# Performance work log

Hardware: AMD Instinct MI355X
Metric: run time of the kernel (lower is better)

The kernel has to match this reference:

```python
import jax, jax.numpy as jnp
import numpy as np

N = 50000
D = 256
E = 800000


def setup_inputs() -> dict:
    key = jax.random.key(0)
    ks = jax.random.split(key, 9)
    X = jax.random.normal(ks[0], (N, D), dtype=jnp.float32)
    edge_index = jax.random.randint(ks[1], (2, E), 0, N, dtype=jnp.int32)
    edge_weight = jax.random.uniform(ks[2], (E,), dtype=jnp.float32)
    p = jax.random.normal(ks[3], (D,), dtype=jnp.float32)
    s = 1.0 / np.sqrt(D)
    W_ih = jax.random.normal(ks[4], (3 * D, D), dtype=jnp.float32) * s
    W_hh = jax.random.normal(ks[5], (3 * D, D), dtype=jnp.float32) * s
    b_ih = jax.random.normal(ks[6], (3 * D,), dtype=jnp.float32) * s
    b_hh = jax.random.normal(ks[7], (3 * D,), dtype=jnp.float32) * s
    W0 = jax.random.normal(ks[8], (D, D), dtype=jnp.float32) * s
    return {"X": X, "edge_index": edge_index, "edge_weight": edge_weight,
            "p": p, "W_ih": W_ih, "W_hh": W_hh, "b_ih": b_ih, "b_hh": b_hh, "W0": W0}


def reference(X, edge_index, edge_weight, p, W_ih, W_hh, b_ih, b_hh, W0):
    n, d = X.shape  # n=N, d=D; ratio = d/n -> TopK keeps k=d nodes
    k = d

    # ---- TopKPooling: score = X.p/||p||, keep top-k, gate by tanh(score) ----
    score = X @ p / jnp.linalg.norm(p)          # [n]
    top_score, idx = jax.lax.top_k(score, k)    # [k]
    x_tilde = X[idx] * jnp.tanh(top_score)[:, None]  # [k, d]

    # ---- Single-step GRU: input x_tilde (batch=k=d), hidden = conv weight W0 [d,d] ----
    h = W0
    gi = x_tilde @ W_ih.T + b_ih                # [d, 3d]
    gh = h @ W_hh.T + b_hh                      # [d, 3d]
    i_r, i_z, i_n = jnp.split(gi, 3, axis=1)
    h_r, h_z, h_n = jnp.split(gh, 3, axis=1)
    r = jax.nn.sigmoid(i_r + h_r)
    z = jax.nn.sigmoid(i_z + h_z)
    nn_ = jnp.tanh(i_n + r * h_n)
    W_new = (1.0 - z) * nn_ + z * h             # evolved conv weight [d, d]

    # ---- GCNConv (no bias): x = X @ W, symmetric norm with self-loops ----
    xw = X @ W_new                              # [n, d]
    src, dst = edge_index[0], edge_index[1]
    loop = jnp.arange(n, dtype=src.dtype)
    src_f = jnp.concatenate([src, loop])
    dst_f = jnp.concatenate([dst, loop])
    ew_f = jnp.concatenate([edge_weight, jnp.ones((n,), dtype=X.dtype)])
    deg = jax.ops.segment_sum(ew_f, dst_f, num_segments=n)  # [n]
    dinv = jnp.where(deg > 0, jax.lax.rsqrt(deg), 0.0)
    norm = dinv[src_f] * ew_f * dinv[dst_f]     # [E+n]
    msgs = norm[:, None] * xw[src_f]            # [E+n, d] gather
    out = jax.ops.segment_sum(msgs, dst_f, num_segments=n)  # scatter-add
    return out
```

## Files before the change

### kernel.cpp

```cpp
#include <hip/hip_runtime.h>
#include <cstdint>
#include <cstddef>

#define N_NODES 50000
#define DIM     256
#define NEDGE   800000
#define TOPK    256
#define HBINS   65536
#define CAND_CAP 2048
#define SLOT    64
#define SROWS   32

typedef unsigned long long u64;
typedef float f32x4 __attribute__((ext_vector_type(4)));
typedef __bf16 b16x8 __attribute__((ext_vector_type(8)));
typedef unsigned short us8 __attribute__((ext_vector_type(8)));

__device__ __forceinline__ u64 okey(double d) {
  u64 b = (u64)__double_as_longlong(d);
  return (b & 0x8000000000000000ULL) ? ~b : (b | 0x8000000000000000ULL);
}

__device__ __forceinline__ unsigned short f2bf(float f) {
  unsigned u = __float_as_uint(f);
  return (unsigned short)((u + 0x7fffu + ((u >> 16) & 1u)) >> 16);
}

__device__ __forceinline__ float bf2f(unsigned short u) {
  return __uint_as_float(((unsigned)u) << 16);
}

__global__ __launch_bounds__(256) void init_kernel(unsigned* __restrict__ w, int nwords) {
  int stride = gridDim.x * 256;
  for (int i = blockIdx.x * 256 + threadIdx.x; i < nwords; i += stride) w[i] = 0u;
}

__global__ __launch_bounds__(256) void score_kernel(const float* __restrict__ X,
                             const float* __restrict__ p,
                             double* __restrict__ scores, unsigned* __restrict__ hist) {
  __shared__ double part[SROWS][65];
  int tid = threadIdx.x;
  int lane = tid & 63, wid = tid >> 6;
  float4 p4 = reinterpret_cast<const float4*>(p)[lane];
  int nblk_rows = gridDim.x * SROWS;
  for (int rb = blockIdx.x * SROWS; rb < N_NODES; rb += nblk_rows) {
    int r0 = rb + wid * 8;
    float4 x[8];
#pragma unroll
    for (int u = 0; u < 8; ++u) {
      int r = r0 + u;
      x[u] = (r < N_NODES)
           ? reinterpret_cast<const float4*>(X + (size_t)r * DIM)[lane]
           : make_float4(0.f, 0.f, 0.f, 0.f);
    }
#pragma unroll
    for (int u = 0; u < 8; ++u) {
      double s = (double)x[u].x * p4.x + (double)x[u].y * p4.y +
                 (double)x[u].z * p4.z + (double)x[u].w * p4.w;
      part[wid * 8 + u][lane] = s;
    }
    __syncthreads();
    if (tid < SROWS) {
      int row = rb + tid;
      if (row < N_NODES) {
        const double* pr = part[tid];
        double a0 = 0.0, a1 = 0.0, a2 = 0.0, a3 = 0.0;
#pragma unroll
        for (int l = 0; l < 64; l += 4) {
          a0 += pr[l + 0]; a1 += pr[l + 1]; a2 += pr[l + 2]; a3 += pr[l + 3];
        }
        double s = (a0 + a1) + (a2 + a3);
        scores[row] = s;
        unsigned bin = (unsigned)(okey(s) >> 48);
        atomicAdd(&hist[bin], 1u);
      }
    }
    __syncthreads();
  }
}

__global__ __launch_bounds__(1024) void findbin_kernel(const unsigned* __restrict__ hist,
                                                       int* __restrict__ ctrl) {
  __shared__ int sums[1024];
  int t = threadIdx.x;
  int base = t * 64;
  const uint4* h4 = reinterpret_cast<const uint4*>(hist + base);
  int s = 0;
#pragma unroll
  for (int i = 0; i < 16; ++i) {
    uint4 v = h4[i];
    s += (int)(v.x + v.y + v.z + v.w);
  }
  sums[t] = s;
  __syncthreads();
  for (int off = 1; off < 1024; off <<= 1) {
    int x = (t + off < 1024) ? sums[t + off] : 0;
    __syncthreads();
    sums[t] += x;
    __syncthreads();
  }
  int S_incl = sums[t];
  int S_excl = S_incl - s;
  if (S_excl < TOPK && S_incl >= TOPK) {
    int c = S_excl;
    int thr = base;
    for (int b = base + 63; b >= base; --b) {
      c += (int)hist[b];
      if (c >= TOPK) { thr = b; break; }
    }
    ctrl[0] = thr;
  }
}

__global__ void collect_kernel(const double* __restrict__ scores, int* __restrict__ ctrl,
                               double* __restrict__ cand_s, int* __restrict__ cand_i) {
  int i = blockIdx.x * 256 + threadIdx.x;
  if (i >= N_NODES) return;
  double sc = scores[i];
  int bin = (int)(okey(sc) >> 48);
  if (bin >= ctrl[0]) {
    int pos = atomicAdd(&ctrl[1], 1);
    if (pos < CAND_CAP) { cand_s[pos] = sc; cand_i[pos] = i; }
  }
}

__global__ __launch_bounds__(1024) void sort_kernel(const int* __restrict__ ctrl,
                                                    const double* __restrict__ cand_s,
                                                    const int* __restrict__ cand_i,
                                                    const float* __restrict__ p,
                                                    int* __restrict__ top_idx,
                                                    float* __restrict__ gate) {
  __shared__ double cs[CAND_CAP];
  __shared__ int ci[CAND_CAP];
  __shared__ double pred[256];
  int t = threadIdx.x;
  if (t < 256) {
    double v = (double)p[t];
    pred[t] = v * v;
  }
  int cnt = ctrl[1];
  if (cnt > CAND_CAP) cnt = CAND_CAP;
  int M = (cnt <= 1024) ? 1024 : CAND_CAP;
  for (int s = 0; s < M / 1024; ++s) {
    int i = t + s * 1024;
    if (i < cnt) { cs[i] = cand_s[i]; ci[i] = cand_i[i]; }
    else         { cs[i] = -1e308;    ci[i] = 0x7fffffff; }
  }
  __syncthreads();
  if (t < 128) pred[t] += pred[t + 128];
  __syncthreads();
  if (t < 64) pred[t] += pred[t + 64];
  __syncthreads();
  if (t < 32) { pred[t] += pred[t + 32]; }
  __syncthreads();
  if (t == 0) {
    double acc = 0.0;
    for (int i = 0; i < 32; ++i) acc += pred[i];
    pred[0] = sqrt(acc);
  }
  for (int k2 = 2; k2 <= M; k2 <<= 1) {
    for (int j = k2 >> 1; j > 0; j >>= 1) {
      for (int s = 0; s < M / 1024; ++s) {
        int i = t + s * 1024;
        int ixj = i ^ j;
        if (ixj > i) {
          double si = cs[i], sx = cs[ixj];
          int ii = ci[i], ix = ci[ixj];
          bool up = ((i & k2) == 0);
          bool sw = up ? ((sx > si) || (sx == si && ix < ii))
                       : ((si > sx) || (si == sx && ii < ix));
          if (sw) { cs[i] = sx; cs[ixj] = si; ci[i] = ix; ci[ixj] = ii; }
        }
      }
      __syncthreads();
    }
  }
  if (t < TOPK) {
    top_idx[t] = ci[t];
    gate[t] = (float)tanh(cs[t] / pred[0]);
  }
}

__global__ __launch_bounds__(256) void gru_gemm_kernel(const float* __restrict__ X,
                                const int* __restrict__ top_idx, const float* __restrict__ gate,
                                const float* __restrict__ W0,
                                const float* __restrict__ W_ih, const float* __restrict__ W_hh,
                                const float* __restrict__ b_ih, const float* __restrict__ b_hh,
                                float* __restrict__ gi, float* __restrict__ gh) {
  __shared__ float As[8][DIM];
  int tid = threadIdx.x;
  int c = blockIdx.x * 256 + tid;
  int r0 = blockIdx.y * 8;
  int which = blockIdx.z;
  const float* W = which ? W_hh : W_ih;
  const float* b = which ? b_hh : b_ih;
  float* outp = which ? gh : gi;
  if (which) {
    const float4* src = reinterpret_cast<const float4*>(W0 + (size_t)r0 * DIM);
    float4* dst = reinterpret_cast<float4*>(&As[0][0]);
    dst[tid] = src[tid];
    dst[tid + 256] = src[tid + 256];
  } else {
#pragma unroll
    for (int h = 0; h < 2; ++h) {
      int idx2 = tid + h * 256;
      int r = idx2 >> 6;
      int e = idx2 & 63;
      int srcrow = top_idx[r0 + r];
      float g = gate[r0 + r];
      float4 v = reinterpret_cast<const float4*>(X + (size_t)srcrow * DIM)[e];
      v.x *= g; v.y *= g; v.z *= g; v.w *= g;
      reinterpret_cast<float4*>(&As[0][0])[idx2] = v;
    }
  }
  __syncthreads();
  const float4* Wr = reinterpret_cast<const float4*>(W + (size_t)c * DIM);
  float acc[8] = {0, 0, 0, 0, 0, 0, 0, 0};
#pragma unroll 4
  for (int k4 = 0; k4 < DIM / 4; ++k4) {
    float4 w = Wr[k4];
#pragma unroll
    for (int r = 0; r < 8; ++r) {
      acc[r] += As[r][k4 * 4 + 0] * w.x + As[r][k4 * 4 + 1] * w.y +
                As[r][k4 * 4 + 2] * w.z + As[r][k4 * 4 + 3] * w.w;
    }
  }
  float bc = b[c];
#pragma unroll
  for (int r = 0; r < 8; ++r)
    outp[(size_t)(r0 + r) * 768 + c] = acc[r] + bc;
}

__global__ void wnew_kernel(const float* __restrict__ gi, const float* __restrict__ gh,
                            const float* __restrict__ W0, unsigned short* __restrict__ Wnbt) {
  int rr = blockIdx.x, c = threadIdx.x;
  const float* gir = gi + (size_t)rr * 768;
  const float* ghr = gh + (size_t)rr * 768;
  float i_r = gir[c],       h_r = ghr[c];
  float i_z = gir[c + 256], h_z = ghr[c + 256];
  float i_n = gir[c + 512], h_n = ghr[c + 512];
  float r = 1.f / (1.f + expf(-(i_r + h_r)));
  float z = 1.f / (1.f + expf(-(i_z + h_z)));
  float nn = tanhf(i_n + r * h_n);
  float h = W0[(size_t)rr * DIM + c];
  float w = (1.f - z) * nn + z * h;
  Wnbt[(size_t)c * DIM + rr] = f2bf(w);
}

__global__ __launch_bounds__(256) void xw_mfma_kernel(const float* __restrict__ X,
                                                      const unsigned short* __restrict__ Wnbt,
                                                      unsigned short* __restrict__ xwb) {
  int wid = threadIdx.x >> 6, lane = threadIdx.x & 63;
  int r0 = blockIdx.x * 64 + wid * 16;
  if (r0 >= N_NODES) return;
  int rowA = r0 + (lane & 15);
  int kgrp = lane >> 4;
  int koff = kgrp * 8;

  const float4* Ar = reinterpret_cast<const float4*>(X + (size_t)rowA * DIM);
  b16x8 afr[8];
#pragma unroll
  for (int kt = 0; kt < 8; ++kt) {
    float4 f0 = Ar[kt * 8 + kgrp * 2 + 0];
    float4 f1 = Ar[kt * 8 + kgrp * 2 + 1];
    union { us8 u; b16x8 b; } cv;
    cv.u[0] = f2bf(f0.x); cv.u[1] = f2bf(f0.y); cv.u[2] = f2bf(f0.z); cv.u[3] = f2bf(f0.w);
    cv.u[4] = f2bf(f1.x); cv.u[5] = f2bf(f1.y); cv.u[6] = f2bf(f1.z); cv.u[7] = f2bf(f1.w);
    afr[kt] = cv.b;
  }

  int colB = lane & 15;
  const unsigned short* Bbase = Wnbt + (size_t)colB * DIM + koff;
  int rr = r0 + kgrp * 4;
#pragma unroll 4
  for (int nf = 0; nf < 16; ++nf) {
    f32x4 acc = {0.f, 0.f, 0.f, 0.f};
    const unsigned short* Bp = Bbase + (size_t)nf * 16 * DIM;
#pragma unroll
    for (int kt = 0; kt < 8; ++kt) {
      b16x8 bfr = *reinterpret_cast<const b16x8*>(Bp + kt * 32);
      acc = __builtin_amdgcn_mfma_f32_16x16x32_bf16(afr[kt], bfr, acc, 0, 0, 0);
    }
    int cc = nf * 16 + colB;
#pragma unroll
    for (int j = 0; j < 4; ++j)
      xwb[(size_t)(rr + j) * DIM + cc] = f2bf(acc[j]);
  }
}

__global__ __launch_bounds__(256) void scatter_kernel(const int* __restrict__ ei,
                               const float* __restrict__ ew,
                               float* __restrict__ deg,
                               int* __restrict__ fill, u64* __restrict__ colval) {
  int stride = gridDim.x * 256;
  for (int e = blockIdx.x * 256 + threadIdx.x; e < NEDGE; e += stride) {
    int s = ei[e], d = ei[NEDGE + e];
    float w = ew[e];
    atomicAdd(&deg[d], w);
    int pos = atomicAdd(&fill[d], 1);
    if (pos < SLOT)
      colval[(size_t)d * SLOT + pos] = ((u64)__float_as_uint(w) << 32) | (unsigned)s;
  }
}

__global__ __launch_bounds__(256) void agg_kernel(const unsigned short* __restrict__ xwb,
                           const float* __restrict__ deg,
                           const int* __restrict__ fill, const u64* __restrict__ colval,
                           float* __restrict__ out) {
  int lane = threadIdx.x & 63;
  int gw = blockIdx.x * 4 + (threadIdx.x >> 6);
  int nw = gridDim.x * 4;
  for (int i = gw; i < N_NODES; i += nw) {
    float di = __frsqrt_rn(deg[i] + 1.0f);
    ushort4 sv = reinterpret_cast<const ushort4*>(xwb + (size_t)i * DIM)[lane];
    float4 acc;
    acc.x = di * bf2f(sv.x); acc.y = di * bf2f(sv.y);
    acc.z = di * bf2f(sv.z); acc.w = di * bf2f(sv.w);
    int n = fill[i];
    if (n > SLOT) n = SLOT;
    const u64* cv = colval + (size_t)i * SLOT;
    int j = 0;
    for (; j + 8 <= n; j += 8) {
      u64 a[8];
#pragma unroll
      for (int u = 0; u < 8; ++u) a[u] = cv[j + u];
      unsigned c[8];
      ushort4 m[8];
      float dg[8];
#pragma unroll
      for (int u = 0; u < 8; ++u) {
        c[u] = (unsigned)a[u];
        m[u] = reinterpret_cast<const ushort4*>(xwb + (size_t)c[u] * DIM)[lane];
        dg[u] = deg[c[u]];
      }
#pragma unroll
      for (int u = 0; u < 8; ++u) {
        float v = __uint_as_float((unsigned)(a[u] >> 32)) * __frsqrt_rn(dg[u] + 1.0f);
        acc.x += v * bf2f(m[u].x); acc.y += v * bf2f(m[u].y);
        acc.z += v * bf2f(m[u].z); acc.w += v * bf2f(m[u].w);
      }
    }
    for (; j < n; ++j) {
      u64 a0 = cv[j];
      unsigned c0 = (unsigned)a0;
      ushort4 m0 = reinterpret_cast<const ushort4*>(xwb + (size_t)c0 * DIM)[lane];
      float v0 = __uint_as_float((unsigned)(a0 >> 32)) * __frsqrt_rn(deg[c0] + 1.0f);
      acc.x += v0 * bf2f(m0.x); acc.y += v0 * bf2f(m0.y);
      acc.z += v0 * bf2f(m0.z); acc.w += v0 * bf2f(m0.w);
    }
    acc.x *= di; acc.y *= di; acc.z *= di; acc.w *= di;
    reinterpret_cast<float4*>(out + (size_t)i * DIM)[lane] = acc;
  }
}

extern "C" void kernel_launch(void* const* d_in, const int* in_sizes, int n_in,
                              void* d_out, int out_size, void* d_ws, size_t ws_size,
                              hipStream_t stream) {
  const float* X    = (const float*)d_in[0];
  const int*   ei   = (const int*)d_in[1];
  const float* ew   = (const float*)d_in[2];
  const float* p    = (const float*)d_in[3];
  const float* W_ih = (const float*)d_in[4];
  const float* W_hh = (const float*)d_in[5];
  const float* b_ih = (const float*)d_in[6];
  const float* b_hh = (const float*)d_in[7];
  const float* W0   = (const float*)d_in[8];
  float* out = (float*)d_out;

  char* ws = (char*)d_ws;
  size_t off = 0;
  auto alloc = [&](size_t bytes) { size_t o = off; off = (off + bytes + 255) & ~(size_t)255; return o; };

  size_t hist_o  = alloc(HBINS * 4);
  size_t ctrl_o  = alloc(64);
  size_t deg_o   = alloc(N_NODES * 4);
  size_t fill_o  = alloc(N_NODES * 4);
  size_t zero_span = off;
  size_t scores_o = alloc(N_NODES * 8);
  size_t cands_o  = alloc(CAND_CAP * 8);
  size_t candi_o  = alloc(CAND_CAP * 4);
  size_t topidx_o = alloc(TOPK * 4);
  size_t gate_o   = alloc(TOPK * 4);
  size_t gi_o     = alloc((size_t)256 * 768 * 4);
  size_t gh_o     = alloc((size_t)256 * 768 * 4);
  size_t wnbt_o   = alloc((size_t)DIM * DIM * 2);
  size_t colval_o = alloc((size_t)N_NODES * SLOT * 8);
  size_t xwb_o    = alloc((size_t)N_NODES * DIM * 2);
  (void)ws_size; (void)n_in; (void)in_sizes; (void)out_size;

  unsigned* hist  = (unsigned*)(ws + hist_o);
  int*    ctrl    = (int*)(ws + ctrl_o);
  float*  deg     = (float*)(ws + deg_o);
  int*    fill    = (int*)(ws + fill_o);
  double* scores  = (double*)(ws + scores_o);
  double* cand_s  = (double*)(ws + cands_o);
  int*    cand_i  = (int*)(ws + candi_o);
  int*    top_idx = (int*)(ws + topidx_o);
  float*  gate    = (float*)(ws + gate_o);
  float*  gi      = (float*)(ws + gi_o);
  float*  gh      = (float*)(ws + gh_o);
  unsigned short* Wnbt = (unsigned short*)(ws + wnbt_o);
  u64*    colval  = (u64*)(ws + colval_o);
  unsigned short* xwb = (unsigned short*)(ws + xwb_o);

  init_kernel<<<256, 256, 0, stream>>>((unsigned*)ws, (int)(zero_span / 4));
  score_kernel<<<391, 256, 0, stream>>>(X, p, scores, hist);
  findbin_kernel<<<1, 1024, 0, stream>>>(hist, ctrl);
  collect_kernel<<<(N_NODES + 255) / 256, 256, 0, stream>>>(scores, ctrl, cand_s, cand_i);
  sort_kernel<<<1, 1024, 0, stream>>>(ctrl, cand_s, cand_i, p, top_idx, gate);
  gru_gemm_kernel<<<dim3(3, 32, 2), 256, 0, stream>>>(X, top_idx, gate, W0, W_ih, W_hh,
                                                      b_ih, b_hh, gi, gh);
  wnew_kernel<<<256, 256, 0, stream>>>(gi, gh, W0, Wnbt);
  xw_mfma_kernel<<<(N_NODES + 63) / 64, 256, 0, stream>>>(X, Wnbt, xwb);
  scatter_kernel<<<1024, 256, 0, stream>>>(ei, ew, deg, fill, colval);
  agg_kernel<<<2048, 256, 0, stream>>>(xwb, deg, fill, colval, out);
}
```

Measured before the change: 434.1 us.

## Replace fixed-slot adjacency with CSR built by count, scan and place

```diff
diff --git a/kernel.cpp b/kernel.cpp
--- a/kernel.cpp
+++ b/kernel.cpp
@@ -8,7 +8,6 @@
 #define TOPK    256
 #define HBINS   65536
 #define CAND_CAP 2048
-#define SLOT    64
 #define SROWS   32
 
 typedef unsigned long long u64;
@@ -288,24 +287,73 @@
   }
 }
 
-__global__ __launch_bounds__(256) void scatter_kernel(const int* __restrict__ ei,
+__global__ __launch_bounds__(256) void count_kernel(const int* __restrict__ ei,
                                const float* __restrict__ ew,
-                               float* __restrict__ deg,
-                               int* __restrict__ fill, u64* __restrict__ colval) {
+                               float* __restrict__ deg, int* __restrict__ cnt) {
+  int stride = gridDim.x * 256;
+  for (int e = blockIdx.x * 256 + threadIdx.x; e < NEDGE; e += stride) {
+    int d = ei[NEDGE + e];
+    atomicAdd(&deg[d], ew[e]);
+    atomicAdd(&cnt[d], 1);
+  }
+}
+
+__global__ __launch_bounds__(1024) void scan1_kernel(const int* __restrict__ cnt,
+                                                     int* __restrict__ rowptr,
+                                                     int* __restrict__ bsum) {
+  __shared__ int sd[1024];
+  int t = threadIdx.x;
+  int i = blockIdx.x * 1024 + t;
+  int v = (i < N_NODES) ? cnt[i] : 0;
+  sd[t] = v;
+  __syncthreads();
+  for (int off = 1; off < 1024; off <<= 1) {
+    int x = (t >= off) ? sd[t - off] : 0;
+    __syncthreads();
+    sd[t] += x;
+    __syncthreads();
+  }
+  if (i < N_NODES) rowptr[i] = sd[t] - v;
+  if (t == 1023) bsum[blockIdx.x] = sd[1023];
+}
+
+__global__ void scan2_kernel(int* __restrict__ bsum, int nb) {
+  int l = threadIdx.x;
+  int orig = (l < nb) ? bsum[l] : 0;
+  int v = orig;
+  for (int off = 1; off < 64; off <<= 1) {
+    int x = __shfl_up(v, off, 64);
+    if (l >= off) v += x;
+  }
+  if (l < nb) bsum[l] = v - orig;
+  if (l == nb - 1) bsum[63] = v;
+}
+
+__global__ __launch_bounds__(1024) void scan3_kernel(int* __restrict__ rowptr,
+                                                     const int* __restrict__ bsum) {
+  int i = blockIdx.x * 1024 + threadIdx.x;
+  int add = bsum[blockIdx.x];
+  if (i < N_NODES) rowptr[i] += add;
+  if (i == 0) rowptr[N_NODES] = bsum[63];
+}
+
+__global__ __launch_bounds__(256) void place_kernel(const int* __restrict__ ei,
+                               const float* __restrict__ ew,
+                               const int* __restrict__ rowptr,
+                               int* __restrict__ fill2, u64* __restrict__ colval) {
   int stride = gridDim.x * 256;
   for (int e = blockIdx.x * 256 + threadIdx.x; e < NEDGE; e += stride) {
     int s = ei[e], d = ei[NEDGE + e];
     float w = ew[e];
-    atomicAdd(&deg[d], w);
-    int pos = atomicAdd(&fill[d], 1);
-    if (pos < SLOT)
-      colval[(size_t)d * SLOT + pos] = ((u64)__float_as_uint(w) << 32) | (unsigned)s;
+    int pos = rowptr[d] + atomicAdd(&fill2[d], 1);
+    colval[pos] = ((u64)__float_as_uint(w) << 32) | (unsigned)s;
   }
 }
 
 __global__ __launch_bounds__(256) void agg_kernel(const unsigned short* __restrict__ xwb,
                            const float* __restrict__ deg,
-                           const int* __restrict__ fill, const u64* __restrict__ colval,
+                           const int* __restrict__ rowptr, const int* __restrict__ cnt,
+                           const u64* __restrict__ colval,
                            float* __restrict__ out) {
   int lane = threadIdx.x & 63;
   int gw = blockIdx.x * 4 + (threadIdx.x >> 6);
@@ -313,12 +361,11 @@
   for (int i = gw; i < N_NODES; i += nw) {
     float di = __frsqrt_rn(deg[i] + 1.0f);
     ushort4 sv = reinterpret_cast<const ushort4*>(xwb + (size_t)i * DIM)[lane];
-    float4 acc;
+    f32x4 acc;
     acc.x = di * bf2f(sv.x); acc.y = di * bf2f(sv.y);
     acc.z = di * bf2f(sv.z); acc.w = di * bf2f(sv.w);
-    int n = fill[i];
-    if (n > SLOT) n = SLOT;
-    const u64* cv = colval + (size_t)i * SLOT;
+    int n = cnt[i];
+    const u64* cv = colval + rowptr[i];
     int j = 0;
     for (; j + 8 <= n; j += 8) {
       u64 a[8];
@@ -349,7 +396,7 @@
       acc.z += v0 * bf2f(m0.z); acc.w += v0 * bf2f(m0.w);
     }
     acc.x *= di; acc.y *= di; acc.z *= di; acc.w *= di;
-    reinterpret_cast<float4*>(out + (size_t)i * DIM)[lane] = acc;
+    __builtin_nontemporal_store(acc, reinterpret_cast<f32x4*>(out + (size_t)i * DIM) + lane);
   }
 }
 
@@ -374,7 +421,8 @@
   size_t hist_o  = alloc(HBINS * 4);
   size_t ctrl_o  = alloc(64);
   size_t deg_o   = alloc(N_NODES * 4);
-  size_t fill_o  = alloc(N_NODES * 4);
+  size_t cnt_o   = alloc(N_NODES * 4);
+  size_t fill2_o = alloc(N_NODES * 4);
   size_t zero_span = off;
   size_t scores_o = alloc(N_NODES * 8);
   size_t cands_o  = alloc(CAND_CAP * 8);
@@ -384,14 +432,17 @@
   size_t gi_o     = alloc((size_t)256 * 768 * 4);
   size_t gh_o     = alloc((size_t)256 * 768 * 4);
   size_t wnbt_o   = alloc((size_t)DIM * DIM * 2);
-  size_t colval_o = alloc((size_t)N_NODES * SLOT * 8);
+  size_t bsum_o   = alloc(64 * 4);
+  size_t rowptr_o = alloc((size_t)(N_NODES + 1) * 4);
+  size_t colval_o = alloc((size_t)NEDGE * 8);
   size_t xwb_o    = alloc((size_t)N_NODES * DIM * 2);
   (void)ws_size; (void)n_in; (void)in_sizes; (void)out_size;
 
   unsigned* hist  = (unsigned*)(ws + hist_o);
   int*    ctrl    = (int*)(ws + ctrl_o);
   float*  deg     = (float*)(ws + deg_o);
-  int*    fill    = (int*)(ws + fill_o);
+  int*    cnt     = (int*)(ws + cnt_o);
+  int*    fill2   = (int*)(ws + fill2_o);
   double* scores  = (double*)(ws + scores_o);
   double* cand_s  = (double*)(ws + cands_o);
   int*    cand_i  = (int*)(ws + candi_o);
@@ -400,8 +451,12 @@
   float*  gi      = (float*)(ws + gi_o);
   float*  gh      = (float*)(ws + gh_o);
   unsigned short* Wnbt = (unsigned short*)(ws + wnbt_o);
+  int*    bsum    = (int*)(ws + bsum_o);
+  int*    rowptr  = (int*)(ws + rowptr_o);
   u64*    colval  = (u64*)(ws + colval_o);
   unsigned short* xwb = (unsigned short*)(ws + xwb_o);
+
+  const int SCAN_NB = (N_NODES + 1023) / 1024;
 
   init_kernel<<<256, 256, 0, stream>>>((unsigned*)ws, (int)(zero_span / 4));
   score_kernel<<<391, 256, 0, stream>>>(X, p, scores, hist);
@@ -412,6 +467,10 @@
                                                       b_ih, b_hh, gi, gh);
   wnew_kernel<<<256, 256, 0, stream>>>(gi, gh, W0, Wnbt);
   xw_mfma_kernel<<<(N_NODES + 63) / 64, 256, 0, stream>>>(X, Wnbt, xwb);
-  scatter_kernel<<<1024, 256, 0, stream>>>(ei, ew, deg, fill, colval);
-  agg_kernel<<<2048, 256, 0, stream>>>(xwb, deg, fill, colval, out);
-}
+  count_kernel<<<1024, 256, 0, stream>>>(ei, ew, deg, cnt);
+  scan1_kernel<<<SCAN_NB, 1024, 0, stream>>>(cnt, rowptr, bsum);
+  scan2_kernel<<<1, 64, 0, stream>>>(bsum, SCAN_NB);
+  scan3_kernel<<<SCAN_NB, 1024, 0, stream>>>(rowptr, bsum);
+  place_kernel<<<1024, 256, 0, stream>>>(ei, ew, rowptr, fill2, colval);
+  agg_kernel<<<2048, 256, 0, stream>>>(xwb, deg, rowptr, cnt, colval, out);
+}
```

Result: slower. 485.7 us (+11.9%).
